# Kernel tuning notes

Measured on AMD Instinct MI355X. Metric: run time of the kernel, lower is better.

## Reference

```python
import jax, jax.numpy as jnp
import numpy as np

FEA = 14      # feature_scal
OUT = 7       # adaptive pool output size
SCALE = 1.0 / 16.0


def _axis_weights(start, end, size):
    """Adaptive-avg-pool weights along one axis for a slice [start, end).
    Matches torch AdaptiveAvgPool1d bin edges: s_i = floor(i*L/OUT),
    e_i = ceil((i+1)*L/OUT). Returns [OUT, size] averaging matrix."""
    i = jnp.arange(OUT)
    length = end - start
    s = start + (i * length) // OUT
    e = start + ((i + 1) * length + (OUT - 1)) // OUT  # ceil div
    pos = jnp.arange(size)
    m = (pos[None, :] >= s[:, None]) & (pos[None, :] < e[:, None])
    denom = jnp.maximum(e - s, 1).astype(jnp.float32)
    return m.astype(jnp.float32) / denom[:, None]


def setup_inputs() -> dict:
    key = jax.random.key(0)
    k1, k2, k3, k4, k5 = jax.random.split(key, 5)
    B, C, N = 1, 2048, 512
    tensor = jax.random.normal(k1, (B, C, FEA, FEA), dtype=jnp.float32)
    # ROI rows: [batch_idx, x1, y1, x2, y2] in 224x224 image pixels
    x1 = jax.random.uniform(k2, (N,), minval=0.0, maxval=120.0)
    y1 = jax.random.uniform(k3, (N,), minval=0.0, maxval=120.0)
    w = jax.random.uniform(k4, (N,), minval=32.0, maxval=100.0)
    h = jax.random.uniform(k5, (N,), minval=32.0, maxval=100.0)
    x2 = jnp.minimum(x1 + w, 224.0)
    y2 = jnp.minimum(y1 + h, 224.0)
    ROI = jnp.stack([jnp.zeros((N,)), x1, y1, x2, y2], axis=1).astype(jnp.float32)
    return {"tensor": tensor, "ROI": ROI}


def reference(tensor, ROI):
    # Scale coords to feature-map space; floor/clip starts, ceil/clip ends
    c = ROI[:, 1:] * SCALE  # [N,4] = x1,y1,x2,y2
    x1 = jnp.clip(jnp.floor(c[:, 0]), 0, FEA).astype(jnp.int32)
    y1 = jnp.clip(jnp.floor(c[:, 1]), 0, FEA).astype(jnp.int32)
    x2 = jnp.clip(jnp.ceil(c[:, 2]), 0, FEA).astype(jnp.int32)
    y2 = jnp.clip(jnp.ceil(c[:, 3]), 0, FEA).astype(jnp.int32)
    Wy = jax.vmap(lambda a, b: _axis_weights(a, b, FEA))(y1, y2)  # [N,7,H]
    Wx = jax.vmap(lambda a, b: _axis_weights(a, b, FEA))(x1, x2)  # [N,7,W]
    # pooled[n,b,c,i,j] = sum_{y,x} Wy[n,i,y] * tensor[b,c,y,x] * Wx[n,j,x]
    out = jnp.einsum('niy,bcyx,njx->nbcij', Wy, tensor, Wx)
    N, B, C = out.shape[:3]
    return out.reshape(N * B, C, OUT, OUT)
```

## Files before the change

### kernel.cpp

```cpp
#include <hip/hip_runtime.h>

#define FEA   14
#define OUT   7
#define SCALE (1.0f / 16.0f)
#define BLK   256
#define CMAX  7
#define CPAD  197
#define GROUPS 16

typedef float fvec4 __attribute__((ext_vector_type(4)));

__device__ __forceinline__ float inv_small(int d) {
    return (d <= 1) ? 1.0f : ((d == 2) ? 0.5f : 0.33333334f);
}

#define C7P 0.14295714f
#define C7M 0.14275714f

__global__ __launch_bounds__(BLK) void roi_adaptive_pool_kernel(
    const float* __restrict__ tensor,
    const float* __restrict__ ROI,
    float* __restrict__ out,
    int C, int N)
{
    __shared__ float sin_[CMAX * CPAD];

    const int tid   = threadIdx.x;
    const int o0    = blockIdx.x * BLK;
    const int total = C * OUT * OUT;

    const int c_lo = o0 / 49;
    const int c_hi = min((o0 + BLK - 1) / 49, C - 1);
    const int nf4  = (c_hi - c_lo + 1) * 49;
    const fvec4* __restrict__ g4 = (const fvec4*)(tensor + (size_t)c_lo * (FEA * FEA));
    for (int t = tid; t < nf4; t += BLK) {
        fvec4 v = g4[t];
        const int f   = t * 4;
        const int cl  = f / 196;
        const int off = f - cl * 196;
        float* p = &sin_[cl * CPAD + off];
        p[0] = v.x; p[1] = v.y; p[2] = v.z; p[3] = v.w;
    }

    const int oi = o0 + tid;
    const bool active = (oi < total);
    const int c  = active ? (oi / 49) : c_lo;
    const int r  = oi - c * 49;
    const int i  = r / 7;
    const int j  = r - i * 7;
    const int lbase = (c - c_lo) * CPAD;
    const float jP  = (float)j       * C7P;
    const float j1M = (float)(j + 1) * C7M;
    const float iP  = (float)i       * C7P;
    const float i1M = (float)(i + 1) * C7M;

    __syncthreads();
    if (!active) return;

    const int n0    = blockIdx.y * ((N + GROUPS - 1) / GROUPS);
    const int n_end = min(n0 + (N + GROUPS - 1) / GROUPS, N);
    if (n0 >= N) return;

    float rx1 = ROI[(size_t)n0 * 5 + 1], ry1 = ROI[(size_t)n0 * 5 + 2];
    float rx2 = ROI[(size_t)n0 * 5 + 3], ry2 = ROI[(size_t)n0 * 5 + 4];
    float* __restrict__ outp = out + (size_t)n0 * total + oi;

    for (int n = n0; n < n_end; ++n) {
        const float x1f = floorf(rx1 * SCALE);
        const float y1f = floorf(ry1 * SCALE);
        const float x2f = ceilf (rx2 * SCALE);
        const float y2f = ceilf (ry2 * SCALE);
        if (n + 1 < n_end) {
            const float* __restrict__ rp = &ROI[(size_t)(n + 1) * 5];
            rx1 = rp[1]; ry1 = rp[2]; rx2 = rp[3]; ry2 = rp[4];
        }
        const float Lxf = x2f - x1f;
        const float Lyf = y2f - y1f;
        const int x1i = (int)x1f, y1i = (int)y1f;

        const int sx = x1i + (int)(jP  * Lxf);
        const int ex = x1i + (int)ceilf(j1M * Lxf);
        const int sy = y1i + (int)(iP  * Lyf);
        const int ey = y1i + (int)ceilf(i1M * Lyf);
        const float w = inv_small(ex - sx) * inv_small(ey - sy);

        float acc = 0.f;
        for (int y = sy; y < ey; ++y) {
            const float* __restrict__ row = &sin_[lbase + y * FEA];
            for (int x = sx; x < ex; ++x) acc += row[x];
        }
        __builtin_nontemporal_store(acc * w, outp);
        outp += total;
    }
}

extern "C" void kernel_launch(void* const* d_in, const int* in_sizes, int n_in,
                              void* d_out, int out_size, void* d_ws, size_t ws_size,
                              hipStream_t stream) {
    const float* tensor = (const float*)d_in[0];
    const float* ROI    = (const float*)d_in[1];
    float*       out    = (float*)d_out;

    const int C = in_sizes[0] / (FEA * FEA);
    const int N = in_sizes[1] / 5;

    const int total = C * OUT * OUT;
    dim3 block(BLK, 1, 1);
    dim3 grid((total + BLK - 1) / BLK, GROUPS, 1);
    roi_adaptive_pool_kernel<<<grid, block, 0, stream>>>(tensor, ROI, out, C, N);
}
```

Measured before the change: 252.0 us.

## Replace per-bin window summation with shared-memory summed-area table lookups

Each block now builds a 2D prefix-sum (integral image) of its channels in LDS, doing a row scan and then a column scan. Each output bin then takes four lookups instead of a variable-length nested loop over up to 3x3 cells. This removes the data-dependent loop and its divergence from the per-ROI inner loop. In exchange, staging uses scalar row loads instead of float4 loads, adds an extra barrier, and prefix-sum subtraction can change float rounding slightly.

New measurement: 232.2 us. 1.09x faster.

```diff
diff --git a/kernel.cpp b/kernel.cpp
--- a/kernel.cpp
+++ b/kernel.cpp
@@ -1,21 +1,20 @@
 #include <hip/hip_runtime.h>
 
-#define FEA   14
-#define OUT   7
-#define SCALE (1.0f / 16.0f)
-#define BLK   256
-#define CMAX  7
-#define CPAD  197
+#define FEA    14
+#define OUT    7
+#define SCALE  (1.0f / 16.0f)
+#define BLK    256
+#define CMAX   7
+#define RS     17
+#define CH     (15 * RS)
 #define GROUPS 16
 
-typedef float fvec4 __attribute__((ext_vector_type(4)));
+#define C7P 0.14295714f
+#define C7M 0.14275714f
 
 __device__ __forceinline__ float inv_small(int d) {
     return (d <= 1) ? 1.0f : ((d == 2) ? 0.5f : 0.33333334f);
 }
-
-#define C7P 0.14295714f
-#define C7M 0.14275714f
 
 __global__ __launch_bounds__(BLK) void roi_adaptive_pool_kernel(
     const float* __restrict__ tensor,
@@ -23,7 +22,7 @@
     float* __restrict__ out,
     int C, int N)
 {
-    __shared__ float sin_[CMAX * CPAD];
+    __shared__ float S[CMAX * CH];
 
     const int tid   = threadIdx.x;
     const int o0    = blockIdx.x * BLK;
@@ -31,39 +30,61 @@
 
     const int c_lo = o0 / 49;
     const int c_hi = min((o0 + BLK - 1) / 49, C - 1);
-    const int nf4  = (c_hi - c_lo + 1) * 49;
-    const fvec4* __restrict__ g4 = (const fvec4*)(tensor + (size_t)c_lo * (FEA * FEA));
-    for (int t = tid; t < nf4; t += BLK) {
-        fvec4 v = g4[t];
-        const int f   = t * 4;
-        const int cl  = f / 196;
-        const int off = f - cl * 196;
-        float* p = &sin_[cl * CPAD + off];
-        p[0] = v.x; p[1] = v.y; p[2] = v.z; p[3] = v.w;
+    const int cnt  = c_hi - c_lo + 1;
+
+    if (tid < CMAX * FEA) {
+        const int cl = tid / FEA;
+        const int y  = tid - cl * FEA;
+        if (cl < cnt) {
+            const float* __restrict__ g =
+                tensor + (size_t)(c_lo + cl) * (FEA * FEA) + y * FEA;
+            float* __restrict__ s = &S[cl * CH + (y + 1) * RS];
+            s[0] = 0.f;
+            float run = 0.f;
+#pragma unroll
+            for (int x = 0; x < FEA; ++x) { run += g[x]; s[x + 1] = run; }
+        }
+    } else if (tid < CMAX * FEA + CMAX * 15) {
+        const int t2 = tid - CMAX * FEA;
+        const int cl = t2 / 15;
+        const int x  = t2 - cl * 15;
+        if (cl < cnt) S[cl * CH + x] = 0.f;
+    }
+    __syncthreads();
+
+    if (tid < CMAX * FEA) {
+        const int cl = tid / FEA;
+        const int x  = (tid - cl * FEA) + 1;
+        if (cl < cnt) {
+            float* __restrict__ s = &S[cl * CH + x];
+            float run = 0.f;
+#pragma unroll
+            for (int y = 1; y <= FEA; ++y) { run += s[y * RS]; s[y * RS] = run; }
+        }
     }
 
     const int oi = o0 + tid;
     const bool active = (oi < total);
     const int c  = active ? (oi / 49) : c_lo;
-    const int r  = oi - c * 49;
-    const int i  = r / 7;
-    const int j  = r - i * 7;
-    const int lbase = (c - c_lo) * CPAD;
+    const int rr = active ? (oi - c * 49) : 0;
+    const int i  = rr / 7;
+    const int j  = rr - i * 7;
+    const int sb = (c - c_lo) * CH;
     const float jP  = (float)j       * C7P;
     const float j1M = (float)(j + 1) * C7M;
     const float iP  = (float)i       * C7P;
     const float i1M = (float)(i + 1) * C7M;
 
     __syncthreads();
-    if (!active) return;
 
-    const int n0    = blockIdx.y * ((N + GROUPS - 1) / GROUPS);
-    const int n_end = min(n0 + (N + GROUPS - 1) / GROUPS, N);
-    if (n0 >= N) return;
+    const int per   = (N + GROUPS - 1) / GROUPS;
+    const int n0    = blockIdx.y * per;
+    const int n_end = min(n0 + per, N);
+    if (n0 >= n_end) return;
 
+    float* __restrict__ outp = out + (size_t)n0 * total + oi;
     float rx1 = ROI[(size_t)n0 * 5 + 1], ry1 = ROI[(size_t)n0 * 5 + 2];
     float rx2 = ROI[(size_t)n0 * 5 + 3], ry2 = ROI[(size_t)n0 * 5 + 4];
-    float* __restrict__ outp = out + (size_t)n0 * total + oi;
 
     for (int n = n0; n < n_end; ++n) {
         const float x1f = floorf(rx1 * SCALE);
@@ -78,18 +99,17 @@
         const float Lyf = y2f - y1f;
         const int x1i = (int)x1f, y1i = (int)y1f;
 
-        const int sx = x1i + (int)(jP  * Lxf);
+        const int sx = x1i + (int)(jP * Lxf);
         const int ex = x1i + (int)ceilf(j1M * Lxf);
-        const int sy = y1i + (int)(iP  * Lyf);
+        const int sy = y1i + (int)(iP * Lyf);
         const int ey = y1i + (int)ceilf(i1M * Lyf);
         const float w = inv_small(ex - sx) * inv_small(ey - sy);
 
-        float acc = 0.f;
-        for (int y = sy; y < ey; ++y) {
-            const float* __restrict__ row = &sin_[lbase + y * FEA];
-            for (int x = sx; x < ex; ++x) acc += row[x];
-        }
-        __builtin_nontemporal_store(acc * w, outp);
+        const float* __restrict__ Sy0 = &S[sb + sy * RS];
+        const float* __restrict__ Sy1 = &S[sb + ey * RS];
+        const float acc = (Sy1[ex] - Sy0[ex]) - (Sy1[sx] - Sy0[sx]);
+
+        if (active) __builtin_nontemporal_store(acc * w, outp);
         outp += total;
     }
 }
```
